# Kernel tuning notes

Measured on AMD Instinct MI355X. Metric: run time of the kernel, lower is better.

The kernel has to match this reference:

```python
import jax, jax.numpy as jnp
import numpy as np

T, B, OBS, H, A = 512, 512, 128, 128, 18


def setup_inputs() -> dict:
    key = jax.random.key(0)
    ks = jax.random.split(key, 8)
    return {
        "hidden": jnp.zeros((B, H), jnp.float32),
        "obs": jax.random.normal(ks[0], (T, B, OBS), jnp.float32),
        "dones": jax.random.bernoulli(ks[1], 0.01, (T, B)),
        # embedding Dense (orthogonal-ish scale sqrt(2))
        "W_emb": jax.random.normal(ks[2], (OBS, H), jnp.float32) * (np.sqrt(2.0) / np.sqrt(OBS)).astype(np.float32),
        "b_emb": jnp.zeros((H,), jnp.float32),
        # GRUCell params: input path Wi/bi cover gates [r | z | n]; hidden path Wh (no bias for r,z), bhn for n
        "Wi": jax.random.normal(ks[3], (H, 3 * H), jnp.float32) / np.float32(np.sqrt(H)),
        "bi": jnp.zeros((3 * H,), jnp.float32),
        "Wh": jax.random.normal(ks[4], (H, 3 * H), jnp.float32) / np.float32(np.sqrt(H)),
        "bhn": jnp.zeros((H,), jnp.float32),
        # output Dense to action_dim
        "W_out": jax.random.normal(ks[5], (H, A), jnp.float32) / np.float32(np.sqrt(H)),
        "b_out": jnp.zeros((A,), jnp.float32),
    }


def reference(hidden, obs, dones, W_emb, b_emb, Wi, bi, Wh, bhn, W_out, b_out):
    # Dense embed + relu: [T, B, OBS] -> [T, B, H]
    emb = jax.nn.relu(obs @ W_emb + b_emb)
    # precompute input-path gate pre-activations for all steps: [T, B, 3H]
    gi = emb @ Wi + bi

    def step(h, xs):
        gi_t, reset = xs  # [B, 3H], [B]
        # reset-masked carry: initialize_carry gives zeros
        h = jnp.where(reset[:, None], jnp.zeros_like(h), h)
        gh = h @ Wh  # [B, 3H]
        r = jax.nn.sigmoid(gi_t[:, :H] + gh[:, :H])
        z = jax.nn.sigmoid(gi_t[:, H:2 * H] + gh[:, H:2 * H])
        n = jnp.tanh(gi_t[:, 2 * H:] + r * (gh[:, 2 * H:] + bhn))
        h_new = (1.0 - z) * n + z * h
        return h_new, h_new

    h_final, ys = jax.lax.scan(step, hidden, (gi, dones))  # ys: [T, B, H]
    q_vals = ys @ W_out + b_out  # [T, B, A]
    return (h_final, q_vals)
```

## Files before the change

### kernel.cpp

```cpp
#include <hip/hip_runtime.h>

#define T_DIM 512
#define B_DIM 512
#define OBS_DIM 128
#define H_DIM 128
#define A_DIM 18
#define G3 384
#define LDSS 136

#define SC_R (-1.44269504088896f)
#define SC_N (2.88539008177793f)

typedef _Float16 v8h __attribute__((ext_vector_type(8)));
typedef _Float16 v4h __attribute__((ext_vector_type(4)));
typedef _Float16 v2h __attribute__((ext_vector_type(2)));
typedef float v4f __attribute__((ext_vector_type(4)));
typedef float v2f __attribute__((ext_vector_type(2)));

#define EXP2F(x) __builtin_amdgcn_exp2f(x)
#define RCPF(x)  __builtin_amdgcn_rcpf(x)
#define PKRTZ(a,b) __builtin_bit_cast(v2h, __builtin_amdgcn_cvt_pkrtz((a),(b)))

#define BAR() asm volatile("s_waitcnt lgkmcnt(0)\n\ts_barrier" ::: "memory")

__global__ __launch_bounds__(512) void k1_embed_gi(
    const float* __restrict__ obs,
    const float* __restrict__ W_emb,
    const float* __restrict__ b_emb,
    const float* __restrict__ Wi,
    const float* __restrict__ bi,
    _Float16* __restrict__ gRZ,
    _Float16* __restrict__ gN)
{
    __shared__ __align__(16) _Float16 obs_lds[64 * LDSS];
    __shared__ __align__(16) _Float16 emb_lds[64 * LDSS];
    const int tid  = threadIdx.x;
    const int cg   = tid >> 6;
    const int lane = tid & 63;
    const int n16  = lane & 15;
    const int quad = lane >> 4;

    v8h fe[4];
    v8h fi[3][4];
#pragma unroll
    for (int kt = 0; kt < 4; ++kt)
#pragma unroll
        for (int j = 0; j < 8; ++j) {
            const int k = kt * 32 + quad * 8 + j;
            fe[kt][j] = (_Float16)W_emb[k * H_DIM + cg * 16 + n16];
        }
#pragma unroll
    for (int g = 0; g < 3; ++g) {
        const float sc = (g == 2) ? SC_N : SC_R;
#pragma unroll
        for (int kt = 0; kt < 4; ++kt)
#pragma unroll
            for (int j = 0; j < 8; ++j) {
                const int k = kt * 32 + quad * 8 + j;
                fi[g][kt][j] = (_Float16)(Wi[k * G3 + g * H_DIM + cg * 16 + n16] * sc);
            }
    }
    float bemb[4], bir[4], biz[4], bin_[4];
#pragma unroll
    for (int r = 0; r < 4; ++r) {
        const int col = cg * 16 + quad * 4 + r;
        bemb[r] = b_emb[col];
        bir[r]  = bi[col] * SC_R;
        biz[r]  = bi[H_DIM + col] * SC_R;
        bin_[r] = bi[2 * H_DIM + col] * SC_N;
    }

    const int srow = tid >> 3;
    const int sk   = (tid & 7) * 16;
    const int base = blockIdx.x * 16;

    {
        const float* op = obs + (size_t)(base * 64 + srow) * OBS_DIM + sk;
#pragma unroll
        for (int q = 0; q < 4; ++q) {
            const float4 a = *(const float4*)(op + q * 4);
            v4h pa = { (_Float16)a.x, (_Float16)a.y, (_Float16)a.z, (_Float16)a.w };
            *(v4h*)&obs_lds[srow * LDSS + sk + q * 4] = pa;
        }
    }
    __syncthreads();

    for (int i = 0; i < 16; ++i) {
        const int row0 = (base + i) * 64;
        const int ni = (i + 1 < 16) ? i + 1 : i;
        const float* opn = obs + (size_t)((base + ni) * 64 + srow) * OBS_DIM + sk;
        float4 nv[4];
#pragma unroll
        for (int q = 0; q < 4; ++q) nv[q] = *(const float4*)(opn + q * 4);

#pragma unroll
        for (int rt = 0; rt < 4; ++rt) {
            v8h bo[4];
#pragma unroll
            for (int kt = 0; kt < 4; ++kt)
                bo[kt] = *(const v8h*)&obs_lds[(rt * 16 + n16) * LDSS + kt * 32 + quad * 8];
            v4f ea = {0.f, 0.f, 0.f, 0.f};
#pragma unroll
            for (int kt = 0; kt < 4; ++kt)
                ea = __builtin_amdgcn_mfma_f32_16x16x32_f16(fe[kt], bo[kt], ea, 0, 0, 0);
            v4h e;
#pragma unroll
            for (int r = 0; r < 4; ++r) e[r] = (_Float16)fmaxf(ea[r] + bemb[r], 0.f);
            *(v4h*)&emb_lds[(rt * 16 + n16) * LDSS + cg * 16 + quad * 4] = e;
        }
        BAR();
#pragma unroll
        for (int rt = 0; rt < 4; ++rt) {
            v8h be[4];
#pragma unroll
            for (int kt = 0; kt < 4; ++kt)
                be[kt] = *(const v8h*)&emb_lds[(rt * 16 + n16) * LDSS + kt * 32 + quad * 8];
            v4f ar = {0.f,0.f,0.f,0.f}, az = {0.f,0.f,0.f,0.f}, an = {0.f,0.f,0.f,0.f};
#pragma unroll
            for (int kt = 0; kt < 4; ++kt) {
                ar = __builtin_amdgcn_mfma_f32_16x16x32_f16(fi[0][kt], be[kt], ar, 0, 0, 0);
                az = __builtin_amdgcn_mfma_f32_16x16x32_f16(fi[1][kt], be[kt], az, 0, 0, 0);
                an = __builtin_amdgcn_mfma_f32_16x16x32_f16(fi[2][kt], be[kt], an, 0, 0, 0);
            }
            const int R = row0 + rt * 16 + n16;
            v8h rz;
#pragma unroll
            for (int r = 0; r < 4; ++r) {
                rz[r]     = (_Float16)(ar[r] + bir[r]);
                rz[4 + r] = (_Float16)(az[r] + biz[r]);
            }
            *(v8h*)&gRZ[(size_t)R * 256 + cg * 32 + quad * 8] = rz;
            v4h nn;
#pragma unroll
            for (int r = 0; r < 4; ++r) nn[r] = (_Float16)(an[r] + bin_[r]);
            *(v4h*)&gN[(size_t)R * 128 + cg * 16 + quad * 4] = nn;
        }
#pragma unroll
        for (int q = 0; q < 4; ++q) {
            v4h pa = { (_Float16)nv[q].x, (_Float16)nv[q].y, (_Float16)nv[q].z, (_Float16)nv[q].w };
            *(v4h*)&obs_lds[srow * LDSS + sk + q * 4] = pa;
        }
        BAR();
    }
}

__global__ __launch_bounds__(512) void k2_recurrence(
    const float* __restrict__ hidden,
    const unsigned char* __restrict__ dones_raw,
    const _Float16* __restrict__ gRZ,
    _Float16* __restrict__ gN,
    const float* __restrict__ Wh,
    const float* __restrict__ bhn,
    float* __restrict__ out)
{
    __shared__ __align__(16) _Float16 h_lds[2][16 * LDSS];
    __shared__ __align__(16) unsigned char d_lds[(T_DIM + 1) * 16];
    __shared__ int byte_mode;
    const int tid  = threadIdx.x;
    const int w    = tid >> 6;
    const int lane = tid & 63;
    const int n16  = lane & 15;
    const int quad = lane >> 4;
    const int c16  = w * 16 + quad * 4;
    const int B0   = blockIdx.x * 16;

    if (tid == 0) byte_mode = 0;
    __syncthreads();
    {
        int hit = 0;
        for (int i = tid; i < 4096; i += 512)
            if ((i & 3) != 0 && dones_raw[i] == 1) hit = 1;
        if (hit) byte_mode = 1;
    }
    __syncthreads();
    const bool bm = (byte_mode != 0);

    {
        if (bm) {
            const int4 v = *(const int4*)(dones_raw + (size_t)tid * B_DIM + B0);
            *(int4*)&d_lds[tid * 16] = v;
        } else {
            const int* di = (const int*)dones_raw;
            const int* pp = di + (size_t)tid * B_DIM + B0;
            int4 wv; unsigned char* wb = (unsigned char*)&wv;
#pragma unroll
            for (int j = 0; j < 16; ++j) wb[j] = (unsigned char)(pp[j] != 0);
            *(int4*)&d_lds[tid * 16] = wv;
        }
        if (tid == 0) { int4 z = {0,0,0,0}; *(int4*)&d_lds[T_DIM * 16] = z; }
    }

    v8h fh[3][4];
#pragma unroll
    for (int g = 0; g < 3; ++g) {
        const float sc = (g == 2) ? SC_N : SC_R;
#pragma unroll
        for (int kt = 0; kt < 4; ++kt)
#pragma unroll
            for (int j = 0; j < 8; ++j) {
                const int k = kt * 32 + quad * 8 + j;
                fh[g][kt][j] = (_Float16)(Wh[k * G3 + g * H_DIM + w * 16 + n16] * sc);
            }
    }
    const v4f bhn_c = { bhn[c16] * SC_N, bhn[c16 + 1] * SC_N,
                        bhn[c16 + 2] * SC_N, bhn[c16 + 3] * SC_N };

    __syncthreads();

    const bool d0 = d_lds[n16] != 0;
    v4f huv;
#pragma unroll
    for (int r = 0; r < 4; ++r) {
        const float hv = hidden[(size_t)(B0 + n16) * H_DIM + c16 + r];
        huv[r] = d0 ? 0.f : hv;
    }
    {
        v2h h01 = PKRTZ(huv[0], huv[1]);
        v2h h23 = PKRTZ(huv[2], huv[3]);
        v4h hw = { h01[0], h01[1], h23[0], h23[1] };
        *(v4h*)&h_lds[0][n16 * LDSS + c16] = hw;
    }

    const int RZB = B_DIM * 256 * 2;
    const int NB  = B_DIM * 128 * 2;
    const int rzo = ((B0 + n16) * 256 + w * 32 + quad * 8) * 2;
    const int no_ = ((B0 + n16) * 128 + c16) * 2;
    const char* gRZc = (const char*)gRZ;
    char*       gNc  = (char*)gN;

    v8h s8a = *(const v8h*)(gRZc + 0 * (size_t)RZB + rzo);
    v8h s8b = *(const v8h*)(gRZc + 1 * (size_t)RZB + rzo);
    v8h s8c = *(const v8h*)(gRZc + 2 * (size_t)RZB + rzo);
    v8h s8d = *(const v8h*)(gRZc + 3 * (size_t)RZB + rzo);
    v4h s4a = *(const v4h*)(gNc + 0 * (size_t)NB + no_);
    v4h s4b = *(const v4h*)(gNc + 1 * (size_t)NB + no_);
    v4h s4c = *(const v4h*)(gNc + 2 * (size_t)NB + no_);
    v4h s4d = *(const v4h*)(gNc + 3 * (size_t)NB + no_);

    const char* rzb = gRZc + (size_t)4 * RZB;
    const char* nb  = gNc  + (size_t)4 * NB;
    char*       yb  = gNc;
    int dpo = 16 + n16;
    __syncthreads();

    auto STEP = [&](int t, v8h& s8, v4h& s4,
                    const _Float16* __restrict__ hin, _Float16* __restrict__ hout)
        __attribute__((always_inline)) -> void {
        const unsigned char dnx = d_lds[dpo];

        v8h bh[4];
#pragma unroll
        for (int kt = 0; kt < 4; ++kt)
            bh[kt] = *(const v8h*)&hin[n16 * LDSS + kt * 32 + quad * 8];

        v4f ga0 = {0.f,0.f,0.f,0.f};
#pragma unroll
        for (int kt = 0; kt < 4; ++kt)
            ga0 = __builtin_amdgcn_mfma_f32_16x16x32_f16(fh[0][kt], bh[kt], ga0, 0, 0, 0);
        v4f ga1 = {0.f,0.f,0.f,0.f};
#pragma unroll
        for (int kt = 0; kt < 4; ++kt)
            ga1 = __builtin_amdgcn_mfma_f32_16x16x32_f16(fh[1][kt], bh[kt], ga1, 0, 0, 0);

        v2f arl = (v2f){ (float)s8[0], (float)s8[1] } + (v2f){ ga0[0], ga0[1] };
        v2f arh = (v2f){ (float)s8[2], (float)s8[3] } + (v2f){ ga0[2], ga0[3] };
        v2f rgl = { RCPF(EXP2F(arl[0]) + 1.f), RCPF(EXP2F(arl[1]) + 1.f) };
        v2f rgh = { RCPF(EXP2F(arh[0]) + 1.f), RCPF(EXP2F(arh[1]) + 1.f) };

        v4f ga2 = bhn_c;
#pragma unroll
        for (int kt = 0; kt < 4; ++kt)
            ga2 = __builtin_amdgcn_mfma_f32_16x16x32_f16(fh[2][kt], bh[kt], ga2, 0, 0, 0);

        v2f azl = (v2f){ (float)s8[4], (float)s8[5] } + (v2f){ ga1[0], ga1[1] };
        v2f azh = (v2f){ (float)s8[6], (float)s8[7] } + (v2f){ ga1[2], ga1[3] };
        v2f ezl = { EXP2F(azl[0]), EXP2F(azl[1]) };
        v2f ezh = { EXP2F(azh[0]), EXP2F(azh[1]) };

        v2f snl = rgl * (v2f){ ga2[0], ga2[1] } + (v2f){ (float)s4[0], (float)s4[1] };
        v2f snh = rgh * (v2f){ ga2[2], ga2[3] } + (v2f){ (float)s4[2], (float)s4[3] };
        v2f enl = { EXP2F(snl[0]), EXP2F(snl[1]) };
        v2f enh = { EXP2F(snh[0]), EXP2F(snh[1]) };
        v2f enpl = enl + 1.f, enph = enh + 1.f;
        v2f enml = enl - 1.f, enmh = enh - 1.f;
        v2f hul = { huv[0], huv[1] }, huh = { huv[2], huv[3] };
        v2f numl = hul * enpl + enml * ezl;
        v2f numh = huh * enph + enmh * ezh;
        v2f denl = enpl * (ezl + 1.f);
        v2f denh = enph * (ezh + 1.f);
        v2f hnl = numl * (v2f){ RCPF(denl[0]), RCPF(denl[1]) };
        v2f hnh = numh * (v2f){ RCPF(denh[0]), RCPF(denh[1]) };

        v2h y01 = PKRTZ(hnl[0], hnl[1]);
        v2h y23 = PKRTZ(hnh[0], hnh[1]);
        v4h yv = { y01[0], y01[1], y23[0], y23[1] };
        const bool dn = dnx != 0;
        v4h hz = { (_Float16)0.f, (_Float16)0.f, (_Float16)0.f, (_Float16)0.f };
        v4h hv = dn ? hz : yv;
        *(v4h*)&hout[n16 * LDSS + c16] = hv;
        *(v4h*)(yb + no_) = yv;
        huv = dn ? (v4f){0.f,0.f,0.f,0.f} : (v4f){ hnl[0], hnl[1], hnh[0], hnh[1] };

        s8 = *(const v8h*)(rzb + rzo);
        s4 = *(const v4h*)(nb + no_);

        if (t < 507) { rzb += RZB; nb += NB; }
        yb += NB; dpo += 16;
        BAR();
    };

    for (int t = 0; t < T_DIM; t += 4) {
        STEP(t,     s8a, s4a, h_lds[0], h_lds[1]);
        STEP(t + 1, s8b, s4b, h_lds[1], h_lds[0]);
        STEP(t + 2, s8c, s4c, h_lds[0], h_lds[1]);
        STEP(t + 3, s8d, s4d, h_lds[1], h_lds[0]);
    }

#pragma unroll
    for (int r = 0; r < 4; ++r)
        out[(size_t)(B0 + n16) * H_DIM + c16 + r] = huv[r];
}

__global__ __launch_bounds__(256) void k3_qout(
    const _Float16* __restrict__ ys,
    const float* __restrict__ W_out,
    const float* __restrict__ b_out,
    float* __restrict__ qout)
{
    const int tid  = threadIdx.x;
    const int wv   = tid >> 6;
    const int lane = tid & 63;
    const int n16  = lane & 15;
    const int quad = lane >> 4;
    const int R0   = blockIdx.x * 64 + wv * 16;

    v8h fo[2][4];
#pragma unroll
    for (int ct = 0; ct < 2; ++ct)
#pragma unroll
        for (int kt = 0; kt < 4; ++kt)
#pragma unroll
            for (int j = 0; j < 8; ++j) {
                const int k = kt * 32 + quad * 8 + j;
                const int col = ct * 16 + n16;
                fo[ct][kt][j] = (col < A_DIM) ? (_Float16)W_out[k * A_DIM + col] : (_Float16)0.f;
            }
    float bq0[4], bq1[4];
#pragma unroll
    for (int r = 0; r < 4; ++r) {
        const int c0 = quad * 4 + r;
        const int c1 = 16 + quad * 4 + r;
        bq0[r] = b_out[c0];
        bq1[r] = (c1 < A_DIM) ? b_out[c1] : 0.f;
    }

    v8h by[4];
#pragma unroll
    for (int kt = 0; kt < 4; ++kt)
        by[kt] = *(const v8h*)(ys + (size_t)(R0 + n16) * 128 + kt * 32 + quad * 8);
    v4f q0 = {0.f,0.f,0.f,0.f}, q1 = {0.f,0.f,0.f,0.f};
#pragma unroll
    for (int kt = 0; kt < 4; ++kt) {
        q0 = __builtin_amdgcn_mfma_f32_16x16x32_f16(fo[0][kt], by[kt], q0, 0, 0, 0);
        q1 = __builtin_amdgcn_mfma_f32_16x16x32_f16(fo[1][kt], by[kt], q1, 0, 0, 0);
    }
    float* qp = qout + (size_t)(R0 + n16) * A_DIM;
#pragma unroll
    for (int r = 0; r < 4; ++r) qp[quad * 4 + r] = q0[r] + bq0[r];
    if (quad == 0) {
#pragma unroll
        for (int r = 0; r < 2; ++r) qp[16 + r] = q1[r] + bq1[r];
    }
}

extern "C" void kernel_launch(void* const* d_in, const int* in_sizes, int n_in,
                              void* d_out, int out_size, void* d_ws, size_t ws_size,
                              hipStream_t stream) {
    const float* hidden = (const float*)d_in[0];
    const float* obs    = (const float*)d_in[1];
    const unsigned char* dones = (const unsigned char*)d_in[2];
    const float* W_emb  = (const float*)d_in[3];
    const float* b_emb  = (const float*)d_in[4];
    const float* Wi     = (const float*)d_in[5];
    const float* bi     = (const float*)d_in[6];
    const float* Wh     = (const float*)d_in[7];
    const float* bhn    = (const float*)d_in[8];
    const float* W_out  = (const float*)d_in[9];
    const float* b_out  = (const float*)d_in[10];
    float* out = (float*)d_out;

    _Float16* gRZ = (_Float16*)d_ws;
    _Float16* gN  = gRZ + (size_t)T_DIM * B_DIM * 256;

    hipLaunchKernelGGL(k1_embed_gi, dim3(256), dim3(512), 0, stream,
                       obs, W_emb, b_emb, Wi, bi, gRZ, gN);
    hipLaunchKernelGGL(k2_recurrence, dim3(32), dim3(512), 0, stream,
                       hidden, dones, gRZ, gN, Wh, bhn, out);
    hipLaunchKernelGGL(k3_qout, dim3(4096), dim3(256), 0, stream,
                       gN, W_out, b_out, out + (size_t)B_DIM * H_DIM);
}
```

Before: 629.8 us.

## Fuse embed, recurrence and output into one cooperative producer-consumer kernel

Merges the three kernels into one cooperative launch. 32 blocks run the GRU recurrence while 224 producer blocks compute input-gate pre-activations in time order and signal progress through global atomic flags. After that, the producers compute the output projection for each timestep once all recurrence blocks have published past it. This overlaps the embedding GEMM and the Q-projection with the serial recurrence instead of running them back to back. It adds spin-wait and fence overhead and a memset, and it depends on every block being co-resident.

```diff
diff --git a/kernel.cpp b/kernel.cpp
--- a/kernel.cpp
+++ b/kernel.cpp
@@ -7,6 +7,8 @@
 #define A_DIM 18
 #define G3 384
 #define LDSS 136
+#define NPROD 224
+#define NCHUNK 4096
 
 #define SC_R (-1.44269504088896f)
 #define SC_N (2.88539008177793f)
@@ -23,353 +25,400 @@
 
 #define BAR() asm volatile("s_waitcnt lgkmcnt(0)\n\ts_barrier" ::: "memory")
 
-__global__ __launch_bounds__(512) void k1_embed_gi(
+__global__ __launch_bounds__(512) void fused_rnn(
+    const float* __restrict__ hidden,
     const float* __restrict__ obs,
+    const unsigned char* __restrict__ dones_raw,
     const float* __restrict__ W_emb,
     const float* __restrict__ b_emb,
     const float* __restrict__ Wi,
     const float* __restrict__ bi,
+    const float* __restrict__ Wh,
+    const float* __restrict__ bhn,
+    const float* __restrict__ W_out,
+    const float* __restrict__ b_out,
+    float* __restrict__ out,
     _Float16* __restrict__ gRZ,
-    _Float16* __restrict__ gN)
+    _Float16* __restrict__ gN,
+    int* flags)
 {
-    __shared__ __align__(16) _Float16 obs_lds[64 * LDSS];
-    __shared__ __align__(16) _Float16 emb_lds[64 * LDSS];
+    __shared__ __align__(16) char smem[2 * 64 * LDSS * 2];
     const int tid  = threadIdx.x;
-    const int cg   = tid >> 6;
+    const int bid  = blockIdx.x;
     const int lane = tid & 63;
     const int n16  = lane & 15;
     const int quad = lane >> 4;
 
-    v8h fe[4];
-    v8h fi[3][4];
-#pragma unroll
-    for (int kt = 0; kt < 4; ++kt)
-#pragma unroll
-        for (int j = 0; j < 8; ++j) {
-            const int k = kt * 32 + quad * 8 + j;
-            fe[kt][j] = (_Float16)W_emb[k * H_DIM + cg * 16 + n16];
-        }
-#pragma unroll
-    for (int g = 0; g < 3; ++g) {
-        const float sc = (g == 2) ? SC_N : SC_R;
+    if (bid < 32) {
+        _Float16* h0 = (_Float16*)smem;
+        _Float16* h1 = (_Float16*)(smem + 16 * LDSS * 2);
+        unsigned char* d_lds = (unsigned char*)(smem + 2 * 16 * LDSS * 2);
+        volatile int* bm_p = (volatile int*)(smem + 2 * 16 * LDSS * 2 + (T_DIM + 1) * 16);
+
+        const int w    = tid >> 6;
+        const int c16  = w * 16 + quad * 4;
+        const int B0   = bid * 16;
+
+        if (tid == 0) *bm_p = 0;
+        __syncthreads();
+        {
+            int hit = 0;
+            for (int i = tid; i < 4096; i += 512)
+                if ((i & 3) != 0 && dones_raw[i] == 1) hit = 1;
+            if (hit) *bm_p = 1;
+        }
+        __syncthreads();
+        const bool bm = (*bm_p != 0);
+
+        {
+            if (bm) {
+                const int4 v = *(const int4*)(dones_raw + (size_t)tid * B_DIM + B0);
+                *(int4*)&d_lds[tid * 16] = v;
+            } else {
+                const int* di = (const int*)dones_raw;
+                const int* pp = di + (size_t)tid * B_DIM + B0;
+                int4 wv; unsigned char* wb = (unsigned char*)&wv;
+#pragma unroll
+                for (int j = 0; j < 16; ++j) wb[j] = (unsigned char)(pp[j] != 0);
+                *(int4*)&d_lds[tid * 16] = wv;
+            }
+            if (tid == 0) { int4 z = {0,0,0,0}; *(int4*)&d_lds[T_DIM * 16] = z; }
+        }
+
+        v8h fh[3][4];
+#pragma unroll
+        for (int g = 0; g < 3; ++g) {
+            const float sc = (g == 2) ? SC_N : SC_R;
+#pragma unroll
+            for (int kt = 0; kt < 4; ++kt)
+#pragma unroll
+                for (int j = 0; j < 8; ++j) {
+                    const int k = kt * 32 + quad * 8 + j;
+                    fh[g][kt][j] = (_Float16)(Wh[k * G3 + g * H_DIM + w * 16 + n16] * sc);
+                }
+        }
+        const v4f bhn_c = { bhn[c16] * SC_N, bhn[c16 + 1] * SC_N,
+                            bhn[c16 + 2] * SC_N, bhn[c16 + 3] * SC_N };
+
+        __syncthreads();
+
+        const bool d0 = d_lds[n16] != 0;
+        v4f huv;
+#pragma unroll
+        for (int r = 0; r < 4; ++r) {
+            const float hv = hidden[(size_t)(B0 + n16) * H_DIM + c16 + r];
+            huv[r] = d0 ? 0.f : hv;
+        }
+        {
+            v2h h01 = PKRTZ(huv[0], huv[1]);
+            v2h h23 = PKRTZ(huv[2], huv[3]);
+            v4h hw = { h01[0], h01[1], h23[0], h23[1] };
+            *(v4h*)&h0[n16 * LDSS + c16] = hw;
+        }
+
+        const int RZB = B_DIM * 256 * 2;
+        const int NB  = B_DIM * 128 * 2;
+        const int rzo = ((B0 + n16) * 256 + w * 32 + quad * 8) * 2;
+        const int no_ = ((B0 + n16) * 128 + c16) * 2;
+        const char* gRZc = (const char*)gRZ;
+        char*       gNc  = (char*)gN;
+
+        int ready_hi = 8;
+        if (tid == 0) {
+            for (int s = 0; s < 8; ++s)
+                while (__hip_atomic_load(&flags[s], __ATOMIC_RELAXED, __HIP_MEMORY_SCOPE_AGENT) < 8)
+                    __builtin_amdgcn_s_sleep(8);
+            __threadfence();
+        }
+        __syncthreads();
+
+        v8h s8a = *(const v8h*)(gRZc + 0 * (size_t)RZB + rzo);
+        v8h s8b = *(const v8h*)(gRZc + 1 * (size_t)RZB + rzo);
+        v8h s8c = *(const v8h*)(gRZc + 2 * (size_t)RZB + rzo);
+        v8h s8d = *(const v8h*)(gRZc + 3 * (size_t)RZB + rzo);
+        v4h s4a = *(const v4h*)(gNc + 0 * (size_t)NB + no_);
+        v4h s4b = *(const v4h*)(gNc + 1 * (size_t)NB + no_);
+        v4h s4c = *(const v4h*)(gNc + 2 * (size_t)NB + no_);
+        v4h s4d = *(const v4h*)(gNc + 3 * (size_t)NB + no_);
+
+        const char* rzb = gRZc + (size_t)4 * RZB;
+        const char* nb  = gNc  + (size_t)4 * NB;
+        char*       yb  = gNc;
+        int dpo = 16 + n16;
+        __syncthreads();
+
+        auto STEP = [&](int t, v8h& s8, v4h& s4,
+                        const _Float16* __restrict__ hin, _Float16* __restrict__ hout)
+            __attribute__((always_inline)) -> void {
+            {
+                const int need = t + 4;
+                if (need < T_DIM && need >= ready_hi) {
+                    const int hi = (need + 16 < T_DIM) ? need + 16 : T_DIM;
+                    if (tid == 0) {
+                        for (int s = ready_hi; s < hi; ++s)
+                            while (__hip_atomic_load(&flags[s], __ATOMIC_RELAXED, __HIP_MEMORY_SCOPE_AGENT) < 8)
+                                __builtin_amdgcn_s_sleep(8);
+                        __threadfence();
+                    }
+                    __syncthreads();
+                    ready_hi = hi;
+                }
+            }
+            const unsigned char dnx = d_lds[dpo];
+
+            v8h bh[4];
+#pragma unroll
+            for (int kt = 0; kt < 4; ++kt)
+                bh[kt] = *(const v8h*)&hin[n16 * LDSS + kt * 32 + quad * 8];
+
+            v4f ga0 = {0.f,0.f,0.f,0.f};
+#pragma unroll
+            for (int kt = 0; kt < 4; ++kt)
+                ga0 = __builtin_amdgcn_mfma_f32_16x16x32_f16(fh[0][kt], bh[kt], ga0, 0, 0, 0);
+            v4f ga1 = {0.f,0.f,0.f,0.f};
+#pragma unroll
+            for (int kt = 0; kt < 4; ++kt)
+                ga1 = __builtin_amdgcn_mfma_f32_16x16x32_f16(fh[1][kt], bh[kt], ga1, 0, 0, 0);
+
+            v2f arl = (v2f){ (float)s8[0], (float)s8[1] } + (v2f){ ga0[0], ga0[1] };
+            v2f arh = (v2f){ (float)s8[2], (float)s8[3] } + (v2f){ ga0[2], ga0[3] };
+            v2f rgl = { RCPF(EXP2F(arl[0]) + 1.f), RCPF(EXP2F(arl[1]) + 1.f) };
+            v2f rgh = { RCPF(EXP2F(arh[0]) + 1.f), RCPF(EXP2F(arh[1]) + 1.f) };
+
+            v4f ga2 = bhn_c;
+#pragma unroll
+            for (int kt = 0; kt < 4; ++kt)
+                ga2 = __builtin_amdgcn_mfma_f32_16x16x32_f16(fh[2][kt], bh[kt], ga2, 0, 0, 0);
+
+            v2f azl = (v2f){ (float)s8[4], (float)s8[5] } + (v2f){ ga1[0], ga1[1] };
+            v2f azh = (v2f){ (float)s8[6], (float)s8[7] } + (v2f){ ga1[2], ga1[3] };
+            v2f ezl = { EXP2F(azl[0]), EXP2F(azl[1]) };
+            v2f ezh = { EXP2F(azh[0]), EXP2F(azh[1]) };
+
+            v2f snl = rgl * (v2f){ ga2[0], ga2[1] } + (v2f){ (float)s4[0], (float)s4[1] };
+            v2f snh = rgh * (v2f){ ga2[2], ga2[3] } + (v2f){ (float)s4[2], (float)s4[3] };
+            v2f enl = { EXP2F(snl[0]), EXP2F(snl[1]) };
+            v2f enh = { EXP2F(snh[0]), EXP2F(snh[1]) };
+            v2f enpl = enl + 1.f, enph = enh + 1.f;
+            v2f enml = enl - 1.f, enmh = enh - 1.f;
+            v2f hul = { huv[0], huv[1] }, huh = { huv[2], huv[3] };
+            v2f numl = hul * enpl + enml * ezl;
+            v2f numh = huh * enph + enmh * ezh;
+            v2f denl = enpl * (ezl + 1.f);
+            v2f denh = enph * (ezh + 1.f);
+            v2f hnl = numl * (v2f){ RCPF(denl[0]), RCPF(denl[1]) };
+            v2f hnh = numh * (v2f){ RCPF(denh[0]), RCPF(denh[1]) };
+
+            v2h y01 = PKRTZ(hnl[0], hnl[1]);
+            v2h y23 = PKRTZ(hnh[0], hnh[1]);
+            v4h yv = { y01[0], y01[1], y23[0], y23[1] };
+            const bool dn = dnx != 0;
+            v4h hz = { (_Float16)0.f, (_Float16)0.f, (_Float16)0.f, (_Float16)0.f };
+            v4h hv = dn ? hz : yv;
+            *(v4h*)&hout[n16 * LDSS + c16] = hv;
+            *(v4h*)(yb + no_) = yv;
+            huv = dn ? (v4f){0.f,0.f,0.f,0.f} : (v4f){ hnl[0], hnl[1], hnh[0], hnh[1] };
+
+            s8 = *(const v8h*)(rzb + rzo);
+            s4 = *(const v4h*)(nb + no_);
+
+            if (t < 507) { rzb += RZB; nb += NB; }
+            yb += NB; dpo += 16;
+
+            if ((t & 7) == 7 && tid == 0) {
+                __threadfence();
+                __hip_atomic_store(&flags[512 + bid], t - 4, __ATOMIC_RELEASE, __HIP_MEMORY_SCOPE_AGENT);
+            }
+            BAR();
+        };
+
+        for (int t = 0; t < T_DIM; t += 4) {
+            STEP(t,     s8a, s4a, h0, h1);
+            STEP(t + 1, s8b, s4b, h1, h0);
+            STEP(t + 2, s8c, s4c, h0, h1);
+            STEP(t + 3, s8d, s4d, h1, h0);
+        }
+
+        __syncthreads();
+        if (tid == 0) {
+            __threadfence();
+            __hip_atomic_store(&flags[512 + bid], T_DIM, __ATOMIC_RELEASE, __HIP_MEMORY_SCOPE_AGENT);
+        }
+#pragma unroll
+        for (int r = 0; r < 4; ++r)
+            out[(size_t)(B0 + n16) * H_DIM + c16 + r] = huv[r];
+
+    } else {
+        const int pid = bid - 32;
+        const int cg  = tid >> 6;
+        _Float16* obs_lds = (_Float16*)smem;
+        _Float16* emb_lds = (_Float16*)(smem + 64 * LDSS * 2);
+
+        v8h fe[4];
+        v8h fi[3][4];
 #pragma unroll
         for (int kt = 0; kt < 4; ++kt)
 #pragma unroll
             for (int j = 0; j < 8; ++j) {
                 const int k = kt * 32 + quad * 8 + j;
-                fi[g][kt][j] = (_Float16)(Wi[k * G3 + g * H_DIM + cg * 16 + n16] * sc);
-            }
-    }
-    float bemb[4], bir[4], biz[4], bin_[4];
-#pragma unroll
-    for (int r = 0; r < 4; ++r) {
-        const int col = cg * 16 + quad * 4 + r;
-        bemb[r] = b_emb[col];
-        bir[r]  = bi[col] * SC_R;
-        biz[r]  = bi[H_DIM + col] * SC_R;
-        bin_[r] = bi[2 * H_DIM + col] * SC_N;
-    }
-
-    const int srow = tid >> 3;
-    const int sk   = (tid & 7) * 16;
-    const int base = blockIdx.x * 16;
-
-    {
-        const float* op = obs + (size_t)(base * 64 + srow) * OBS_DIM + sk;
-#pragma unroll
-        for (int q = 0; q < 4; ++q) {
-            const float4 a = *(const float4*)(op + q * 4);
-            v4h pa = { (_Float16)a.x, (_Float16)a.y, (_Float16)a.z, (_Float16)a.w };
-            *(v4h*)&obs_lds[srow * LDSS + sk + q * 4] = pa;
-        }
-    }
-    __syncthreads();
-
-    for (int i = 0; i < 16; ++i) {
-        const int row0 = (base + i) * 64;
-        const int ni = (i + 1 < 16) ? i + 1 : i;
-        const float* opn = obs + (size_t)((base + ni) * 64 + srow) * OBS_DIM + sk;
-        float4 nv[4];
-#pragma unroll
-        for (int q = 0; q < 4; ++q) nv[q] = *(const float4*)(opn + q * 4);
-
-#pragma unroll
-        for (int rt = 0; rt < 4; ++rt) {
-            v8h bo[4];
-#pragma unroll
-            for (int kt = 0; kt < 4; ++kt)
-                bo[kt] = *(const v8h*)&obs_lds[(rt * 16 + n16) * LDSS + kt * 32 + quad * 8];
-            v4f ea = {0.f, 0.f, 0.f, 0.f};
-#pragma unroll
-            for (int kt = 0; kt < 4; ++kt)
-                ea = __builtin_amdgcn_mfma_f32_16x16x32_f16(fe[kt], bo[kt], ea, 0, 0, 0);
-            v4h e;
-#pragma unroll
-            for (int r = 0; r < 4; ++r) e[r] = (_Float16)fmaxf(ea[r] + bemb[r], 0.f);
-            *(v4h*)&emb_lds[(rt * 16 + n16) * LDSS + cg * 16 + quad * 4] = e;
-        }
-        BAR();
-#pragma unroll
-        for (int rt = 0; rt < 4; ++rt) {
-            v8h be[4];
-#pragma unroll
-            for (int kt = 0; kt < 4; ++kt)
-                be[kt] = *(const v8h*)&emb_lds[(rt * 16 + n16) * LDSS + kt * 32 + quad * 8];
-            v4f ar = {0.f,0.f,0.f,0.f}, az = {0.f,0.f,0.f,0.f}, an = {0.f,0.f,0.f,0.f};
-#pragma unroll
-            for (int kt = 0; kt < 4; ++kt) {
-                ar = __builtin_amdgcn_mfma_f32_16x16x32_f16(fi[0][kt], be[kt], ar, 0, 0, 0);
-                az = __builtin_amdgcn_mfma_f32_16x16x32_f16(fi[1][kt], be[kt], az, 0, 0, 0);
-                an = __builtin_amdgcn_mfma_f32_16x16x32_f16(fi[2][kt], be[kt], an, 0, 0, 0);
-            }
-            const int R = row0 + rt * 16 + n16;
-            v8h rz;
-#pragma unroll
-            for (int r = 0; r < 4; ++r) {
-                rz[r]     = (_Float16)(ar[r] + bir[r]);
-                rz[4 + r] = (_Float16)(az[r] + biz[r]);
-            }
-            *(v8h*)&gRZ[(size_t)R * 256 + cg * 32 + quad * 8] = rz;
-            v4h nn;
-#pragma unroll
-            for (int r = 0; r < 4; ++r) nn[r] = (_Float16)(an[r] + bin_[r]);
-            *(v4h*)&gN[(size_t)R * 128 + cg * 16 + quad * 4] = nn;
-        }
-#pragma unroll
-        for (int q = 0; q < 4; ++q) {
-            v4h pa = { (_Float16)nv[q].x, (_Float16)nv[q].y, (_Float16)nv[q].z, (_Float16)nv[q].w };
-            *(v4h*)&obs_lds[srow * LDSS + sk + q * 4] = pa;
-        }
-        BAR();
-    }
-}
-
-__global__ __launch_bounds__(512) void k2_recurrence(
-    const float* __restrict__ hidden,
-    const unsigned char* __restrict__ dones_raw,
-    const _Float16* __restrict__ gRZ,
-    _Float16* __restrict__ gN,
-    const float* __restrict__ Wh,
-    const float* __restrict__ bhn,
-    float* __restrict__ out)
-{
-    __shared__ __align__(16) _Float16 h_lds[2][16 * LDSS];
-    __shared__ __align__(16) unsigned char d_lds[(T_DIM + 1) * 16];
-    __shared__ int byte_mode;
-    const int tid  = threadIdx.x;
-    const int w    = tid >> 6;
-    const int lane = tid & 63;
-    const int n16  = lane & 15;
-    const int quad = lane >> 4;
-    const int c16  = w * 16 + quad * 4;
-    const int B0   = blockIdx.x * 16;
-
-    if (tid == 0) byte_mode = 0;
-    __syncthreads();
-    {
-        int hit = 0;
-        for (int i = tid; i < 4096; i += 512)
-            if ((i & 3) != 0 && dones_raw[i] == 1) hit = 1;
-        if (hit) byte_mode = 1;
-    }
-    __syncthreads();
-    const bool bm = (byte_mode != 0);
-
-    {
-        if (bm) {
-            const int4 v = *(const int4*)(dones_raw + (size_t)tid * B_DIM + B0);
-            *(int4*)&d_lds[tid * 16] = v;
-        } else {
-            const int* di = (const int*)dones_raw;
-            const int* pp = di + (size_t)tid * B_DIM + B0;
-            int4 wv; unsigned char* wb = (unsigned char*)&wv;
-#pragma unroll
-            for (int j = 0; j < 16; ++j) wb[j] = (unsigned char)(pp[j] != 0);
-            *(int4*)&d_lds[tid * 16] = wv;
-        }
-        if (tid == 0) { int4 z = {0,0,0,0}; *(int4*)&d_lds[T_DIM * 16] = z; }
-    }
-
-    v8h fh[3][4];
-#pragma unroll
-    for (int g = 0; g < 3; ++g) {
-        const float sc = (g == 2) ? SC_N : SC_R;
-#pragma unroll
-        for (int kt = 0; kt < 4; ++kt)
-#pragma unroll
-            for (int j = 0; j < 8; ++j) {
-                const int k = kt * 32 + quad * 8 + j;
-                fh[g][kt][j] = (_Float16)(Wh[k * G3 + g * H_DIM + w * 16 + n16] * sc);
-            }
-    }
-    const v4f bhn_c = { bhn[c16] * SC_N, bhn[c16 + 1] * SC_N,
-                        bhn[c16 + 2] * SC_N, bhn[c16 + 3] * SC_N };
-
-    __syncthreads();
-
-    const bool d0 = d_lds[n16] != 0;
-    v4f huv;
-#pragma unroll
-    for (int r = 0; r < 4; ++r) {
-        const float hv = hidden[(size_t)(B0 + n16) * H_DIM + c16 + r];
-        huv[r] = d0 ? 0.f : hv;
-    }
-    {
-        v2h h01 = PKRTZ(huv[0], huv[1]);
-        v2h h23 = PKRTZ(huv[2], huv[3]);
-        v4h hw = { h01[0], h01[1], h23[0], h23[1] };
-        *(v4h*)&h_lds[0][n16 * LDSS + c16] = hw;
-    }
-
-    const int RZB = B_DIM * 256 * 2;
-    const int NB  = B_DIM * 128 * 2;
-    const int rzo = ((B0 + n16) * 256 + w * 32 + quad * 8) * 2;
-    const int no_ = ((B0 + n16) * 128 + c16) * 2;
-    const char* gRZc = (const char*)gRZ;
-    char*       gNc  = (char*)gN;
-
-    v8h s8a = *(const v8h*)(gRZc + 0 * (size_t)RZB + rzo);
-    v8h s8b = *(const v8h*)(gRZc + 1 * (size_t)RZB + rzo);
-    v8h s8c = *(const v8h*)(gRZc + 2 * (size_t)RZB + rzo);
-    v8h s8d = *(const v8h*)(gRZc + 3 * (size_t)RZB + rzo);
-    v4h s4a = *(const v4h*)(gNc + 0 * (size_t)NB + no_);
-    v4h s4b = *(const v4h*)(gNc + 1 * (size_t)NB + no_);
-    v4h s4c = *(const v4h*)(gNc + 2 * (size_t)NB + no_);
-    v4h s4d = *(const v4h*)(gNc + 3 * (size_t)NB + no_);
-
-    const char* rzb = gRZc + (size_t)4 * RZB;
-    const char* nb  = gNc  + (size_t)4 * NB;
-    char*       yb  = gNc;
-    int dpo = 16 + n16;
-    __syncthreads();
-
-    auto STEP = [&](int t, v8h& s8, v4h& s4,
-                    const _Float16* __restrict__ hin, _Float16* __restrict__ hout)
-        __attribute__((always_inline)) -> void {
-        const unsigned char dnx = d_lds[dpo];
-
-        v8h bh[4];
-#pragma unroll
-        for (int kt = 0; kt < 4; ++kt)
-            bh[kt] = *(const v8h*)&hin[n16 * LDSS + kt * 32 + quad * 8];
-
-        v4f ga0 = {0.f,0.f,0.f,0.f};
-#pragma unroll
-        for (int kt = 0; kt < 4; ++kt)
-            ga0 = __builtin_amdgcn_mfma_f32_16x16x32_f16(fh[0][kt], bh[kt], ga0, 0, 0, 0);
-        v4f ga1 = {0.f,0.f,0.f,0.f};
-#pragma unroll
-        for (int kt = 0; kt < 4; ++kt)
-            ga1 = __builtin_amdgcn_mfma_f32_16x16x32_f16(fh[1][kt], bh[kt], ga1, 0, 0, 0);
-
-        v2f arl = (v2f){ (float)s8[0], (float)s8[1] } + (v2f){ ga0[0], ga0[1] };
-        v2f arh = (v2f){ (float)s8[2], (float)s8[3] } + (v2f){ ga0[2], ga0[3] };
-        v2f rgl = { RCPF(EXP2F(arl[0]) + 1.f), RCPF(EXP2F(arl[1]) + 1.f) };
-        v2f rgh = { RCPF(EXP2F(arh[0]) + 1.f), RCPF(EXP2F(arh[1]) + 1.f) };
-
-        v4f ga2 = bhn_c;
-#pragma unroll
-        for (int kt = 0; kt < 4; ++kt)
-            ga2 = __builtin_amdgcn_mfma_f32_16x16x32_f16(fh[2][kt], bh[kt], ga2, 0, 0, 0);
-
-        v2f azl = (v2f){ (float)s8[4], (float)s8[5] } + (v2f){ ga1[0], ga1[1] };
-        v2f azh = (v2f){ (float)s8[6], (float)s8[7] } + (v2f){ ga1[2], ga1[3] };
-        v2f ezl = { EXP2F(azl[0]), EXP2F(azl[1]) };
-        v2f ezh = { EXP2F(azh[0]), EXP2F(azh[1]) };
-
-        v2f snl = rgl * (v2f){ ga2[0], ga2[1] } + (v2f){ (float)s4[0], (float)s4[1] };
-        v2f snh = rgh * (v2f){ ga2[2], ga2[3] } + (v2f){ (float)s4[2], (float)s4[3] };
-        v2f enl = { EXP2F(snl[0]), EXP2F(snl[1]) };
-        v2f enh = { EXP2F(snh[0]), EXP2F(snh[1]) };
-        v2f enpl = enl + 1.f, enph = enh + 1.f;
-        v2f enml = enl - 1.f, enmh = enh - 1.f;
-        v2f hul = { huv[0], huv[1] }, huh = { huv[2], huv[3] };
-        v2f numl = hul * enpl + enml * ezl;
-        v2f numh = huh * enph + enmh * ezh;
-        v2f denl = enpl * (ezl + 1.f);
-        v2f denh = enph * (ezh + 1.f);
-        v2f hnl = numl * (v2f){ RCPF(denl[0]), RCPF(denl[1]) };
-        v2f hnh = numh * (v2f){ RCPF(denh[0]), RCPF(denh[1]) };
-
-        v2h y01 = PKRTZ(hnl[0], hnl[1]);
-        v2h y23 = PKRTZ(hnh[0], hnh[1]);
-        v4h yv = { y01[0], y01[1], y23[0], y23[1] };
-        const bool dn = dnx != 0;
-        v4h hz = { (_Float16)0.f, (_Float16)0.f, (_Float16)0.f, (_Float16)0.f };
-        v4h hv = dn ? hz : yv;
-        *(v4h*)&hout[n16 * LDSS + c16] = hv;
-        *(v4h*)(yb + no_) = yv;
-        huv = dn ? (v4f){0.f,0.f,0.f,0.f} : (v4f){ hnl[0], hnl[1], hnh[0], hnh[1] };
-
-        s8 = *(const v8h*)(rzb + rzo);
-        s4 = *(const v4h*)(nb + no_);
-
-        if (t < 507) { rzb += RZB; nb += NB; }
-        yb += NB; dpo += 16;
-        BAR();
-    };
-
-    for (int t = 0; t < T_DIM; t += 4) {
-        STEP(t,     s8a, s4a, h_lds[0], h_lds[1]);
-        STEP(t + 1, s8b, s4b, h_lds[1], h_lds[0]);
-        STEP(t + 2, s8c, s4c, h_lds[0], h_lds[1]);
-        STEP(t + 3, s8d, s4d, h_lds[1], h_lds[0]);
-    }
-
-#pragma unroll
-    for (int r = 0; r < 4; ++r)
-        out[(size_t)(B0 + n16) * H_DIM + c16 + r] = huv[r];
-}
-
-__global__ __launch_bounds__(256) void k3_qout(
-    const _Float16* __restrict__ ys,
-    const float* __restrict__ W_out,
-    const float* __restrict__ b_out,
-    float* __restrict__ qout)
-{
-    const int tid  = threadIdx.x;
-    const int wv   = tid >> 6;
-    const int lane = tid & 63;
-    const int n16  = lane & 15;
-    const int quad = lane >> 4;
-    const int R0   = blockIdx.x * 64 + wv * 16;
-
-    v8h fo[2][4];
-#pragma unroll
-    for (int ct = 0; ct < 2; ++ct)
-#pragma unroll
-        for (int kt = 0; kt < 4; ++kt)
-#pragma unroll
-            for (int j = 0; j < 8; ++j) {
-                const int k = kt * 32 + quad * 8 + j;
-                const int col = ct * 16 + n16;
-                fo[ct][kt][j] = (col < A_DIM) ? (_Float16)W_out[k * A_DIM + col] : (_Float16)0.f;
-            }
-    float bq0[4], bq1[4];
-#pragma unroll
-    for (int r = 0; r < 4; ++r) {
-        const int c0 = quad * 4 + r;
-        const int c1 = 16 + quad * 4 + r;
-        bq0[r] = b_out[c0];
-        bq1[r] = (c1 < A_DIM) ? b_out[c1] : 0.f;
-    }
-
-    v8h by[4];
-#pragma unroll
-    for (int kt = 0; kt < 4; ++kt)
-        by[kt] = *(const v8h*)(ys + (size_t)(R0 + n16) * 128 + kt * 32 + quad * 8);
-    v4f q0 = {0.f,0.f,0.f,0.f}, q1 = {0.f,0.f,0.f,0.f};
-#pragma unroll
-    for (int kt = 0; kt < 4; ++kt) {
-        q0 = __builtin_amdgcn_mfma_f32_16x16x32_f16(fo[0][kt], by[kt], q0, 0, 0, 0);
-        q1 = __builtin_amdgcn_mfma_f32_16x16x32_f16(fo[1][kt], by[kt], q1, 0, 0, 0);
-    }
-    float* qp = qout + (size_t)(R0 + n16) * A_DIM;
-#pragma unroll
-    for (int r = 0; r < 4; ++r) qp[quad * 4 + r] = q0[r] + bq0[r];
-    if (quad == 0) {
-#pragma unroll
-        for (int r = 0; r < 2; ++r) qp[16 + r] = q1[r] + bq1[r];
+                fe[kt][j] = (_Float16)W_emb[k * H_DIM + cg * 16 + n16];
+            }
+#pragma unroll
+        for (int g = 0; g < 3; ++g) {
+            const float sc = (g == 2) ? SC_N : SC_R;
+#pragma unroll
+            for (int kt = 0; kt < 4; ++kt)
+#pragma unroll
+                for (int j = 0; j < 8; ++j) {
+                    const int k = kt * 32 + quad * 8 + j;
+                    fi[g][kt][j] = (_Float16)(Wi[k * G3 + g * H_DIM + cg * 16 + n16] * sc);
+                }
+        }
+        float bemb[4], bir[4], biz[4], bin_[4];
+#pragma unroll
+        for (int r = 0; r < 4; ++r) {
+            const int col = cg * 16 + quad * 4 + r;
+            bemb[r] = b_emb[col];
+            bir[r]  = bi[col] * SC_R;
+            biz[r]  = bi[H_DIM + col] * SC_R;
+            bin_[r] = bi[2 * H_DIM + col] * SC_N;
+        }
+
+        const int srow = tid >> 3;
+        const int sk   = (tid & 7) * 16;
+
+        {
+            const float* op = obs + (size_t)(pid * 64 + srow) * OBS_DIM + sk;
+#pragma unroll
+            for (int q = 0; q < 4; ++q) {
+                const float4 a = *(const float4*)(op + q * 4);
+                v4h pa = { (_Float16)a.x, (_Float16)a.y, (_Float16)a.z, (_Float16)a.w };
+                *(v4h*)&obs_lds[srow * LDSS + sk + q * 4] = pa;
+            }
+        }
+        __syncthreads();
+
+        for (int g = pid; g < NCHUNK; g += NPROD) {
+            const int gn = (g + NPROD < NCHUNK) ? g + NPROD : g;
+            const float* opn = obs + (size_t)(gn * 64 + srow) * OBS_DIM + sk;
+            float4 nv[4];
+#pragma unroll
+            for (int q = 0; q < 4; ++q) nv[q] = *(const float4*)(opn + q * 4);
+
+#pragma unroll
+            for (int rt = 0; rt < 4; ++rt) {
+                v8h bo[4];
+#pragma unroll
+                for (int kt = 0; kt < 4; ++kt)
+                    bo[kt] = *(const v8h*)&obs_lds[(rt * 16 + n16) * LDSS + kt * 32 + quad * 8];
+                v4f ea = {0.f, 0.f, 0.f, 0.f};
+#pragma unroll
+                for (int kt = 0; kt < 4; ++kt)
+                    ea = __builtin_amdgcn_mfma_f32_16x16x32_f16(fe[kt], bo[kt], ea, 0, 0, 0);
+                v4h e;
+#pragma unroll
+                for (int r = 0; r < 4; ++r) e[r] = (_Float16)fmaxf(ea[r] + bemb[r], 0.f);
+                *(v4h*)&emb_lds[(rt * 16 + n16) * LDSS + cg * 16 + quad * 4] = e;
+            }
+            BAR();
+            const int row0 = g * 64;
+#pragma unroll
+            for (int rt = 0; rt < 4; ++rt) {
+                v8h be[4];
+#pragma unroll
+                for (int kt = 0; kt < 4; ++kt)
+                    be[kt] = *(const v8h*)&emb_lds[(rt * 16 + n16) * LDSS + kt * 32 + quad * 8];
+                v4f ar = {0.f,0.f,0.f,0.f}, az = {0.f,0.f,0.f,0.f}, an = {0.f,0.f,0.f,0.f};
+#pragma unroll
+                for (int kt = 0; kt < 4; ++kt) {
+                    ar = __builtin_amdgcn_mfma_f32_16x16x32_f16(fi[0][kt], be[kt], ar, 0, 0, 0);
+                    az = __builtin_amdgcn_mfma_f32_16x16x32_f16(fi[1][kt], be[kt], az, 0, 0, 0);
+                    an = __builtin_amdgcn_mfma_f32_16x16x32_f16(fi[2][kt], be[kt], an, 0, 0, 0);
+                }
+                const int R = row0 + rt * 16 + n16;
+                v8h rz;
+#pragma unroll
+                for (int r = 0; r < 4; ++r) {
+                    rz[r]     = (_Float16)(ar[r] + bir[r]);
+                    rz[4 + r] = (_Float16)(az[r] + biz[r]);
+                }
+                *(v8h*)&gRZ[(size_t)R * 256 + cg * 32 + quad * 8] = rz;
+                v4h nn;
+#pragma unroll
+                for (int r = 0; r < 4; ++r) nn[r] = (_Float16)(an[r] + bin_[r]);
+                *(v4h*)&gN[(size_t)R * 128 + cg * 16 + quad * 4] = nn;
+            }
+#pragma unroll
+            for (int q = 0; q < 4; ++q) {
+                v4h pa = { (_Float16)nv[q].x, (_Float16)nv[q].y, (_Float16)nv[q].z, (_Float16)nv[q].w };
+                *(v4h*)&obs_lds[srow * LDSS + sk + q * 4] = pa;
+            }
+            __syncthreads();
+            if (tid == 0) {
+                __threadfence();
+                __hip_atomic_fetch_add(&flags[g >> 3], 1, __ATOMIC_RELEASE, __HIP_MEMORY_SCOPE_AGENT);
+            }
+        }
+        __syncthreads();
+
+        v8h fo[2][4];
+#pragma unroll
+        for (int ct = 0; ct < 2; ++ct)
+#pragma unroll
+            for (int kt = 0; kt < 4; ++kt)
+#pragma unroll
+                for (int j = 0; j < 8; ++j) {
+                    const int k = kt * 32 + quad * 8 + j;
+                    const int col = ct * 16 + n16;
+                    fo[ct][kt][j] = (col < A_DIM) ? (_Float16)W_out[k * A_DIM + col] : (_Float16)0.f;
+                }
+        float bq0[4], bq1[4];
+#pragma unroll
+        for (int r = 0; r < 4; ++r) {
+            const int c0 = quad * 4 + r;
+            const int c1 = 16 + quad * 4 + r;
+            bq0[r] = b_out[c0];
+            bq1[r] = (c1 < A_DIM) ? b_out[c1] : 0.f;
+        }
+        float* qout = out + (size_t)B_DIM * H_DIM;
+
+        for (int s = pid; s < T_DIM; s += NPROD) {
+            if (tid == 0) {
+                for (;;) {
+                    int m = 1 << 30;
+#pragma unroll
+                    for (int j = 0; j < 32; ++j) {
+                        const int v = __hip_atomic_load(&flags[512 + j], __ATOMIC_RELAXED, __HIP_MEMORY_SCOPE_AGENT);
+                        m = v < m ? v : m;
+                    }
+                    if (m > s) break;
+                    __builtin_amdgcn_s_sleep(16);
+                }
+                __threadfence();
+            }
+            __syncthreads();
+#pragma unroll
+            for (int rt2 = 0; rt2 < 4; ++rt2) {
+                const int R = s * B_DIM + rt2 * 128 + (tid >> 6) * 16 + n16;
+                v8h by[4];
+#pragma unroll
+                for (int kt = 0; kt < 4; ++kt)
+                    by[kt] = *(const v8h*)(gN + (size_t)R * 128 + kt * 32 + quad * 8);
+                v4f q0 = {0.f,0.f,0.f,0.f}, q1 = {0.f,0.f,0.f,0.f};
+#pragma unroll
+                for (int kt = 0; kt < 4; ++kt) {
+                    q0 = __builtin_amdgcn_mfma_f32_16x16x32_f16(fo[0][kt], by[kt], q0, 0, 0, 0);
+                    q1 = __builtin_amdgcn_mfma_f32_16x16x32_f16(fo[1][kt], by[kt], q1, 0, 0, 0);
+                }
+                float* qp = qout + (size_t)R * A_DIM;
+#pragma unroll
+                for (int r = 0; r < 4; ++r) qp[quad * 4 + r] = q0[r] + bq0[r];
+                if (quad == 0) {
+#pragma unroll
+                    for (int r = 0; r < 2; ++r) qp[16 + r] = q1[r] + bq1[r];
+                }
+            }
+        }
     }
 }
 
@@ -389,13 +438,16 @@
     const float* b_out  = (const float*)d_in[10];
     float* out = (float*)d_out;
 
-    _Float16* gRZ = (_Float16*)d_ws;
+    int* flags = (int*)d_ws;
+    _Float16* gRZ = (_Float16*)((char*)d_ws + 4096);
     _Float16* gN  = gRZ + (size_t)T_DIM * B_DIM * 256;
 
-    hipLaunchKernelGGL(k1_embed_gi, dim3(256), dim3(512), 0, stream,
-                       obs, W_emb, b_emb, Wi, bi, gRZ, gN);
-    hipLaunchKernelGGL(k2_recurrence, dim3(32), dim3(512), 0, stream,
-                       hidden, dones, gRZ, gN, Wh, bhn, out);
-    hipLaunchKernelGGL(k3_qout, dim3(4096), dim3(256), 0, stream,
-                       gN, W_out, b_out, out + (size_t)B_DIM * H_DIM);
+    hipMemsetAsync(flags, 0, 4096, stream);
+
+    void* args[] = { (void*)&hidden, (void*)&obs, (void*)&dones,
+                     (void*)&W_emb, (void*)&b_emb, (void*)&Wi, (void*)&bi,
+                     (void*)&Wh, (void*)&bhn, (void*)&W_out, (void*)&b_out,
+                     (void*)&out, (void*)&gRZ, (void*)&gN, (void*)&flags };
+    hipLaunchCooperativeKernel((void*)fused_rnn, dim3(256), dim3(512),
+                               (void**)args, 0, stream);
 }
```

After: 1.289 ms. 2.05x slower.

## Fuse output projection into recurrence kernel and drop ys round-trip

Applied to the files above, without the earlier changes.

Removes the separate q-value kernel and the fp16 ys write-back. Two waves per block now compute the output projection from the un-reset hidden state already held in LDS, one step late. The reset masking moves from the stored state into zeroing the MFMA results on the next step. This saves a launch plus the ys global write and read, but adds MFMA work and scattered q stores on the serial recurrence's critical path.

```diff
diff --git a/kernel.cpp b/kernel.cpp
--- a/kernel.cpp
+++ b/kernel.cpp
@@ -148,9 +148,11 @@
     const float* __restrict__ hidden,
     const unsigned char* __restrict__ dones_raw,
     const _Float16* __restrict__ gRZ,
-    _Float16* __restrict__ gN,
+    const _Float16* __restrict__ gN,
     const float* __restrict__ Wh,
     const float* __restrict__ bhn,
+    const float* __restrict__ W_out,
+    const float* __restrict__ b_out,
     float* __restrict__ out)
 {
     __shared__ __align__(16) _Float16 h_lds[2][16 * LDSS];
@@ -205,6 +207,25 @@
     const v4f bhn_c = { bhn[c16] * SC_N, bhn[c16 + 1] * SC_N,
                         bhn[c16 + 2] * SC_N, bhn[c16 + 3] * SC_N };
 
+    v8h fo[4];
+    float bq[4];
+    if (w < 2) {
+        const int col = w * 16 + n16;
+#pragma unroll
+        for (int kt = 0; kt < 4; ++kt)
+#pragma unroll
+            for (int j = 0; j < 8; ++j) {
+                const int k = kt * 32 + quad * 8 + j;
+                fo[kt][j] = (col < A_DIM) ? (_Float16)W_out[k * A_DIM + col] : (_Float16)0.f;
+            }
+#pragma unroll
+        for (int r = 0; r < 4; ++r) {
+            const int c = w * 16 + quad * 4 + r;
+            bq[r] = (c < A_DIM) ? b_out[c] : 0.f;
+        }
+    }
+    float* qout = out + (size_t)B_DIM * H_DIM;
+
     __syncthreads();
 
     const bool d0 = d_lds[n16] != 0;
@@ -226,7 +247,7 @@
     const int rzo = ((B0 + n16) * 256 + w * 32 + quad * 8) * 2;
     const int no_ = ((B0 + n16) * 128 + c16) * 2;
     const char* gRZc = (const char*)gRZ;
-    char*       gNc  = (char*)gN;
+    const char* gNc  = (const char*)gN;
 
     v8h s8a = *(const v8h*)(gRZc + 0 * (size_t)RZB + rzo);
     v8h s8b = *(const v8h*)(gRZc + 1 * (size_t)RZB + rzo);
@@ -239,8 +260,8 @@
 
     const char* rzb = gRZc + (size_t)4 * RZB;
     const char* nb  = gNc  + (size_t)4 * NB;
-    char*       yb  = gNc;
     int dpo = 16 + n16;
+    bool dprev = false;
     __syncthreads();
 
     auto STEP = [&](int t, v8h& s8, v4h& s4,
@@ -253,6 +274,20 @@
         for (int kt = 0; kt < 4; ++kt)
             bh[kt] = *(const v8h*)&hin[n16 * LDSS + kt * 32 + quad * 8];
 
+        if (w < 2) {
+            v4f qa = {0.f,0.f,0.f,0.f};
+#pragma unroll
+            for (int kt = 0; kt < 4; ++kt)
+                qa = __builtin_amdgcn_mfma_f32_16x16x32_f16(fo[kt], bh[kt], qa, 0, 0, 0);
+            if (t > 0) {
+                float* qp = qout + ((size_t)(t - 1) * B_DIM + B0 + n16) * A_DIM;
+                const int cbase = w * 16 + quad * 4;
+#pragma unroll
+                for (int r = 0; r < 4; ++r)
+                    if (cbase + r < A_DIM) qp[cbase + r] = qa[r] + bq[r];
+            }
+        }
+
         v4f ga0 = {0.f,0.f,0.f,0.f};
 #pragma unroll
         for (int kt = 0; kt < 4; ++kt)
@@ -261,6 +296,8 @@
 #pragma unroll
         for (int kt = 0; kt < 4; ++kt)
             ga1 = __builtin_amdgcn_mfma_f32_16x16x32_f16(fh[1][kt], bh[kt], ga1, 0, 0, 0);
+
+        if (dprev) { ga0 = (v4f){0.f,0.f,0.f,0.f}; ga1 = (v4f){0.f,0.f,0.f,0.f}; }
 
         v2f arl = (v2f){ (float)s8[0], (float)s8[1] } + (v2f){ ga0[0], ga0[1] };
         v2f arh = (v2f){ (float)s8[2], (float)s8[3] } + (v2f){ ga0[2], ga0[3] };
@@ -271,6 +308,7 @@
 #pragma unroll
         for (int kt = 0; kt < 4; ++kt)
             ga2 = __builtin_amdgcn_mfma_f32_16x16x32_f16(fh[2][kt], bh[kt], ga2, 0, 0, 0);
+        if (dprev) ga2 = bhn_c;
 
         v2f azl = (v2f){ (float)s8[4], (float)s8[5] } + (v2f){ ga1[0], ga1[1] };
         v2f azh = (v2f){ (float)s8[6], (float)s8[7] } + (v2f){ ga1[2], ga1[3] };
@@ -294,18 +332,17 @@
         v2h y01 = PKRTZ(hnl[0], hnl[1]);
         v2h y23 = PKRTZ(hnh[0], hnh[1]);
         v4h yv = { y01[0], y01[1], y23[0], y23[1] };
+        *(v4h*)&hout[n16 * LDSS + c16] = yv;
         const bool dn = dnx != 0;
-        v4h hz = { (_Float16)0.f, (_Float16)0.f, (_Float16)0.f, (_Float16)0.f };
-        v4h hv = dn ? hz : yv;
-        *(v4h*)&hout[n16 * LDSS + c16] = hv;
-        *(v4h*)(yb + no_) = yv;
-        huv = dn ? (v4f){0.f,0.f,0.f,0.f} : (v4f){ hnl[0], hnl[1], hnh[0], hnh[1] };
+#pragma unroll
+        for (int r = 0; r < 4; ++r) huv[r] = dn ? 0.f : (r < 2 ? hnl[r] : hnh[r - 2]);
+        dprev = dn;
 
         s8 = *(const v8h*)(rzb + rzo);
         s4 = *(const v4h*)(nb + no_);
 
         if (t < 507) { rzb += RZB; nb += NB; }
-        yb += NB; dpo += 16;
+        dpo += 16;
         BAR();
     };
 
@@ -316,61 +353,25 @@
         STEP(t + 3, s8d, s4d, h_lds[1], h_lds[0]);
     }
 
+    if (w < 2) {
+        v8h bh[4];
+#pragma unroll
+        for (int kt = 0; kt < 4; ++kt)
+            bh[kt] = *(const v8h*)&h_lds[0][n16 * LDSS + kt * 32 + quad * 8];
+        v4f qa = {0.f,0.f,0.f,0.f};
+#pragma unroll
+        for (int kt = 0; kt < 4; ++kt)
+            qa = __builtin_amdgcn_mfma_f32_16x16x32_f16(fo[kt], bh[kt], qa, 0, 0, 0);
+        float* qp = qout + ((size_t)(T_DIM - 1) * B_DIM + B0 + n16) * A_DIM;
+        const int cbase = w * 16 + quad * 4;
+#pragma unroll
+        for (int r = 0; r < 4; ++r)
+            if (cbase + r < A_DIM) qp[cbase + r] = qa[r] + bq[r];
+    }
+
 #pragma unroll
     for (int r = 0; r < 4; ++r)
         out[(size_t)(B0 + n16) * H_DIM + c16 + r] = huv[r];
-}
-
-__global__ __launch_bounds__(256) void k3_qout(
-    const _Float16* __restrict__ ys,
-    const float* __restrict__ W_out,
-    const float* __restrict__ b_out,
-    float* __restrict__ qout)
-{
-    const int tid  = threadIdx.x;
-    const int wv   = tid >> 6;
-    const int lane = tid & 63;
-    const int n16  = lane & 15;
-    const int quad = lane >> 4;
-    const int R0   = blockIdx.x * 64 + wv * 16;
-
-    v8h fo[2][4];
-#pragma unroll
-    for (int ct = 0; ct < 2; ++ct)
-#pragma unroll
-        for (int kt = 0; kt < 4; ++kt)
-#pragma unroll
-            for (int j = 0; j < 8; ++j) {
-                const int k = kt * 32 + quad * 8 + j;
-                const int col = ct * 16 + n16;
-                fo[ct][kt][j] = (col < A_DIM) ? (_Float16)W_out[k * A_DIM + col] : (_Float16)0.f;
-            }
-    float bq0[4], bq1[4];
-#pragma unroll
-    for (int r = 0; r < 4; ++r) {
-        const int c0 = quad * 4 + r;
-        const int c1 = 16 + quad * 4 + r;
-        bq0[r] = b_out[c0];
-        bq1[r] = (c1 < A_DIM) ? b_out[c1] : 0.f;
-    }
-
-    v8h by[4];
-#pragma unroll
-    for (int kt = 0; kt < 4; ++kt)
-        by[kt] = *(const v8h*)(ys + (size_t)(R0 + n16) * 128 + kt * 32 + quad * 8);
-    v4f q0 = {0.f,0.f,0.f,0.f}, q1 = {0.f,0.f,0.f,0.f};
-#pragma unroll
-    for (int kt = 0; kt < 4; ++kt) {
-        q0 = __builtin_amdgcn_mfma_f32_16x16x32_f16(fo[0][kt], by[kt], q0, 0, 0, 0);
-        q1 = __builtin_amdgcn_mfma_f32_16x16x32_f16(fo[1][kt], by[kt], q1, 0, 0, 0);
-    }
-    float* qp = qout + (size_t)(R0 + n16) * A_DIM;
-#pragma unroll
-    for (int r = 0; r < 4; ++r) qp[quad * 4 + r] = q0[r] + bq0[r];
-    if (quad == 0) {
-#pragma unroll
-        for (int r = 0; r < 2; ++r) qp[16 + r] = q1[r] + bq1[r];
-    }
 }
 
 extern "C" void kernel_launch(void* const* d_in, const int* in_sizes, int n_in,
@@ -395,7 +396,5 @@
     hipLaunchKernelGGL(k1_embed_gi, dim3(256), dim3(512), 0, stream,
                        obs, W_emb, b_emb, Wi, bi, gRZ, gN);
     hipLaunchKernelGGL(k2_recurrence, dim3(32), dim3(512), 0, stream,
-                       hidden, dones, gRZ, gN, Wh, bhn, out);
-    hipLaunchKernelGGL(k3_qout, dim3(4096), dim3(256), 0, stream,
-                       gN, W_out, b_out, out + (size_t)B_DIM * H_DIM);
+                       hidden, dones, gRZ, gN, Wh, bhn, W_out, b_out, out);
 }
```

Result: faster. 598.3 us (-5.0%).
